# Performance work log

Hardware: AMD Instinct MI355X
Metric: run time of the kernel (lower is better)

The kernel has to match this reference:

```python
import jax, jax.numpy as jnp
import numpy as np

B, T, D, M, W = 512, 2048, 32, 64, 128  # batch, times, data_size, model_size, hidden width


def _linwb(key, out_d, in_d):
    kw, kb = jax.random.split(key)
    s = 1.0 / np.sqrt(in_d)
    return (jax.random.uniform(kw, (out_d, in_d), jnp.float32, -s, s),
            jax.random.uniform(kb, (out_d,), jnp.float32, -s, s))


def setup_inputs() -> dict:
    key = jax.random.key(0)
    ks = jax.random.split(key, 9)
    times = jnp.arange(T, dtype=jnp.float32) / T  # increasing, span [0,1)
    xs = 0.1 * jax.random.normal(ks[0], (B, T, D), jnp.float32)
    # encoder MLP: data_size -> 128 -> 128 -> model_size (relu hidden, identity out; eqx defaults)
    enc_W0, enc_b0 = _linwb(ks[1], W, D)
    enc_W1, enc_b1 = _linwb(ks[2], W, W)
    enc_W2, enc_b2 = _linwb(ks[3], M, W)
    # vector field MLP: model_size -> 128 -> 128 -> model_size*data_size (gelu hidden, tanh out)
    vf_W0, vf_b0 = _linwb(ks[4], W, M)
    vf_W1, vf_b1 = _linwb(ks[5], W, W)
    vf_W2, vf_b2 = _linwb(ks[6], M * D, W)
    # decoder: model_size -> 1 (n_classes==2)
    dec_W, dec_b = _linwb(ks[7], 1, M)
    return dict(times=times, xs=xs,
                enc_W0=enc_W0, enc_b0=enc_b0, enc_W1=enc_W1, enc_b1=enc_b1,
                enc_W2=enc_W2, enc_b2=enc_b2,
                vf_W0=vf_W0, vf_b0=vf_b0, vf_W1=vf_W1, vf_b1=vf_b1,
                vf_W2=vf_W2, vf_b2=vf_b2, dec_W=dec_W, dec_b=dec_b)


def reference(times, xs, enc_W0, enc_b0, enc_W1, enc_b1, enc_W2, enc_b2,
              vf_W0, vf_b0, vf_W1, vf_b1, vf_W2, vf_b2, dec_W, dec_b):
    def encoder(x):  # (B, D) -> (B, M)
        h = jax.nn.relu(x @ enc_W0.T + enc_b0)
        h = jax.nn.relu(h @ enc_W1.T + enc_b1)
        return h @ enc_W2.T + enc_b2

    def vf(y):  # (B, M) -> (B, M, D)
        h = jax.nn.gelu(y @ vf_W0.T + vf_b0)
        h = jax.nn.gelu(h @ vf_W1.T + vf_b1)
        h = jnp.tanh(h @ vf_W2.T + vf_b2)
        return h.reshape(y.shape[0], M, D)

    # Linear interpolation control: dX/dt is piecewise constant on each interval.
    dts = times[1:] - times[:-1]                      # (T-1,)
    dxs = jnp.transpose(xs[:, 1:] - xs[:, :-1], (1, 0, 2))  # (T-1, B, D)

    def step(y, inp):
        dt, dx = inp
        dXdt = dx / dt                                # (B, D)

        def g(y_):  # dy/dt = f(y) @ dX/dt
            return jnp.einsum('bmd,bd->bm', vf(y_), dXdt)

        k1 = g(y)
        k2 = g(y + 0.5 * dt * k1)
        k3 = g(y + 0.5 * dt * k2)
        k4 = g(y + dt * k3)
        return y + (dt / 6.0) * (k1 + 2 * k2 + 2 * k3 + k4), None

    y0 = encoder(xs[:, 0])                            # control.evaluate(t0) == xs[:,0]
    yT, _ = jax.lax.scan(step, y0, (dts, dxs))
    logits = yT @ dec_W.T + dec_b                     # (B, 1)
    return jax.nn.sigmoid(logits)
```

## Files before the change

kernel.cpp:

```cpp
#include <hip/hip_runtime.h>


#define TT   2048
#define NTH  512
#define NCH  8
#define R_P  2
#define L_P  2

typedef _Float16 f16;
typedef _Float16 f16x8 __attribute__((ext_vector_type(8)));
typedef float f32x4 __attribute__((ext_vector_type(4)));

#define O_W2L 0
#define O_DTS 131072
#define O_B2  139264
#define O_H1  147456
#define O_H2  151552
#define O_YIN 155648
#define O_GS  157696
#define O_DX  159744
#define O_B0  160768
#define O_B1  161280
#define LDSB  161792

__device__ __forceinline__ float tanh_fast(float x){
    float e = __expf(2.0f * x);
    return 1.0f - 2.0f * __builtin_amdgcn_rcpf(e + 1.0f);
}
__device__ __forceinline__ float gelu_f(float x){
    float u = x + 0.044715f * x * x * x;
    return 0.5f * x * (1.0f + tanh_fast(0.7978845608028654f * u));
}

template<bool F16>
__device__ __forceinline__ void load_tile_frags(f16x8* buf, const f16* w2r,
                                                const float* vW2, int tl, int l){
    if constexpr (F16){
        const f16* base = w2r + (size_t)tl*2048 + l*8;
        #pragma unroll
        for (int kf = 0; kf < 4; ++kf)
            buf[kf] = *(const f16x8*)(base + kf*512);
    } else {
        int n = tl*16 + (l & 15);
        int k0 = (l >> 4) << 3;
        #pragma unroll
        for (int kf = 0; kf < 4; ++kf){
            const float* p = vW2 + n*128 + kf*32 + k0;
            float4 u = *(const float4*)p;
            float4 v2 = *(const float4*)(p + 4);
            f16x8 t;
            t[0]=(f16)u.x; t[1]=(f16)u.y; t[2]=(f16)u.z; t[3]=(f16)u.w;
            t[4]=(f16)v2.x; t[5]=(f16)v2.y; t[6]=(f16)v2.z; t[7]=(f16)v2.w;
            buf[kf] = t;
        }
    }
}

template<bool F16>
__device__ __forceinline__ void issue_pair(f16x8* de, f16x8* dob, const f16* w2r,
                                           const float* vW2, int w, int p, int l){
    if constexpr (F16){
        const f16* be = w2r + ((size_t)(w*16 + 2*p))*2048 + l*8;
        #pragma unroll
        for (int kf = 0; kf < 4; ++kf){
            de[kf]  = *(const f16x8*)(be + kf*512);
            dob[kf] = *(const f16x8*)(be + 2048 + kf*512);
        }
    } else {
        load_tile_frags<false>(de,  nullptr, vW2, w*16 + 2*p,     l);
        load_tile_frags<false>(dob, nullptr, vW2, w*16 + 2*p + 1, l);
    }
}

__global__ void __launch_bounds__(512) reorder_w2(const float* __restrict__ vW2,
                                                  f16* __restrict__ w2r){
    int idx = blockIdx.x * 512 + threadIdx.x;
    int i  = idx & 7;
    int l  = (idx >> 3) & 63;
    int kf = (idx >> 9) & 3;
    int tl = idx >> 11;
    int n = tl*16 + (l & 15);
    int k = kf*32 + ((l >> 4) << 3) + i;
    w2r[idx] = (f16)vW2[n*128 + k];
}

template<bool F16>
__global__ void __launch_bounds__(NTH, 1)
ncde_main(const float* __restrict__ times, const float* __restrict__ xs,
          const float* __restrict__ eW0, const float* __restrict__ eb0,
          const float* __restrict__ eW1, const float* __restrict__ eb1,
          const float* __restrict__ eW2, const float* __restrict__ eb2,
          const float* __restrict__ vW0, const float* __restrict__ vW1,
          const float* __restrict__ vb0, const float* __restrict__ vb1,
          const float* __restrict__ vW2, const float* __restrict__ vb2,
          const float* __restrict__ dW, const float* __restrict__ db,
          const f16* __restrict__ w2r, float* __restrict__ out)
{
    extern __shared__ __align__(16) char lds[];
    float* dtsf = (float*)(lds + O_DTS);
    float* gsf  = (float*)(lds + O_GS);
    float* dxf  = (float*)(lds + O_DX);
    float* b2s  = (float*)(lds + O_B2);
    float* b0f  = (float*)(lds + O_B0);
    float* b1f  = (float*)(lds + O_B1);
    float* enc1f= (float*)(lds + O_H1);
    float* enc2f= (float*)(lds + O_H2);

    const int tid = threadIdx.x;
    const int l   = tid & 63;
    const int w   = tid >> 6;
    const int c0  = blockIdx.x * NCH;

    for (int i = tid; i < 2047; i += NTH) dtsf[i] = times[i+1] - times[i];
    for (int i = tid; i < 2048; i += NTH) b2s[i] = vb2[i];
    if (tid < 128){ b0f[tid] = vb0[tid]; b1f[tid] = vb1[tid]; }

    float xcur = 0.f, xn = 0.f;
    if (tid < 256){
        int r = tid >> 5, d = tid & 31;
        xcur = xs[((size_t)(c0 + r) * TT + 0) * 32 + d];
        xn   = xs[((size_t)(c0 + r) * TT + 1) * 32 + d];
        dxf[r*32 + d] = xcur;
    }
    __syncthreads();

    for (int i = tid; i < NCH*128; i += NTH){
        int r = i >> 7, n = i & 127;
        float a = eb0[n];
        #pragma unroll
        for (int k = 0; k < 32; ++k) a += eW0[n*32 + k] * dxf[r*32 + k];
        enc1f[i] = fmaxf(a, 0.f);
    }
    __syncthreads();
    for (int i = tid; i < NCH*128; i += NTH){
        int r = i >> 7, n = i & 127;
        float a = eb1[n];
        for (int k = 0; k < 128; ++k) a += eW1[n*128 + k] * enc1f[r*128 + k];
        enc2f[i] = fmaxf(a, 0.f);
    }
    __syncthreads();
    float yreg;
    {
        int r = tid >> 6, m = tid & 63;
        float a = eb2[m];
        for (int k = 0; k < 128; ++k) a += eW2[m*128 + k] * enc2f[r*128 + k];
        yreg = a;
    }
    __syncthreads();

    for (int i = tid; i < 10240/4; i += NTH)
        ((unsigned*)(lds + O_H1))[i] = 0u;
    if constexpr (F16){
        for (int i = tid; i < 8192; i += NTH){
            int slot = i >> 8, b = (i & 255) << 4;
            int sw = slot >> 2, sp = (slot >> 1) & 1, se = slot & 1;
            int tl = sw*16 + 2*(R_P + sp) + se;
            *(f16x8*)(lds + O_W2L + slot*4096 + b) =
                *(const f16x8*)((const char*)w2r + (size_t)tl*4096 + b);
        }
    } else {
        for (int i = tid; i < 65536; i += NTH){
            int slot = i >> 11, elem = i & 2047;
            int sw = slot >> 2, sp = (slot >> 1) & 1, se = slot & 1;
            int tl = sw*16 + 2*(R_P + sp) + se;
            int kf = elem >> 9, rem = elem & 511, ll = rem >> 3, ii = rem & 7;
            int n = tl*16 + (ll & 15);
            int k = kf*32 + ((ll >> 4) << 3) + ii;
            *(f16*)(lds + O_W2L + slot*4096 + elem*2) = (f16)vW2[n*128 + k];
        }
    }
    __syncthreads();

    {
        int r = tid >> 6, m = tid & 63;
        *(f16*)(lds + O_YIN + r*128 + ((m*2) ^ ((r & 7) << 4))) = (f16)yreg;
    }

    f16x8 w0f[2], w1f[4];
    {
        int col  = w*16 + (l & 15);
        int krow = (l >> 4) << 3;
        #pragma unroll
        for (int ks = 0; ks < 2; ++ks){
            const float* p = vW0 + col*64 + ks*32 + krow;
            f16x8 v;
            #pragma unroll
            for (int i = 0; i < 8; ++i) v[i] = (f16)p[i];
            w0f[ks] = v;
        }
        #pragma unroll
        for (int ks = 0; ks < 4; ++ks){
            const float* p = vW1 + col*128 + ks*32 + krow;
            f16x8 v;
            #pragma unroll
            for (int i = 0; i < 8; ++i) v[i] = (f16)p[i];
            w1f[ks] = v;
        }
    }
    f16x8 rw2[R_P][2][4];
    #pragma unroll
    for (int p = 0; p < R_P; ++p)
        #pragma unroll
        for (int e = 0; e < 2; ++e)
            load_tile_frags<F16>(rw2[p][e], w2r, vW2, w*16 + 2*p + e, l);
    __syncthreads();

    const int arow = l & 15;
    const int g    = l >> 4;

    for (int t = 0; t < TT-1; ++t){
        float dtv = dtsf[t];
        float xf = 0.f;
        if (tid < 256){
            int r = tid >> 5, d = tid & 31;
            if (t + 2 < TT) xf = xs[((size_t)(c0 + r) * TT + (t+2)) * 32 + d];
            dxf[r*32 + d] = (xn - xcur) / dtv;
            xcur = xn;
        }
        float ka = 0.f;

        #pragma unroll 1
        for (int st = 0; st < 4; ++st){
            f16x8 sAe[4], sAo[4], sBe[4], sBo[4];
            issue_pair<F16>(sAe, sAo, w2r, vW2, w, 4, l);
            issue_pair<F16>(sBe, sBo, w2r, vW2, w, 5, l);

            {
                f32x4 acc = {0.f,0.f,0.f,0.f};
                #pragma unroll
                for (int kf = 0; kf < 2; ++kf){
                    f16x8 a = *(const f16x8*)(lds + O_YIN + arow*128 +
                               ((kf*64 + g*16) ^ ((arow & 7) << 4)));
                    acc = __builtin_amdgcn_mfma_f32_16x16x32_f16(a, w0f[kf], acc, 0, 0, 0);
                }
                if (g < 2){
                    int col = w*16 + (l & 15);
                    float bb = b0f[col];
                    #pragma unroll
                    for (int j = 0; j < 4; ++j){
                        int row = g*4 + j;
                        float gg = gelu_f(acc[j] + bb);
                        *(f16*)(lds + O_H1 + row*256 + ((col*2) ^ ((row & 7) << 4))) = (f16)gg;
                    }
                }
            }
            __syncthreads();
            {
                f32x4 acc = {0.f,0.f,0.f,0.f};
                #pragma unroll
                for (int kf = 0; kf < 4; ++kf){
                    f16x8 a = *(const f16x8*)(lds + O_H1 + arow*256 +
                               ((kf*64 + g*16) ^ ((arow & 7) << 4)));
                    acc = __builtin_amdgcn_mfma_f32_16x16x32_f16(a, w1f[kf], acc, 0, 0, 0);
                }
                if (g < 2){
                    int col = w*16 + (l & 15);
                    float bb = b1f[col];
                    #pragma unroll
                    for (int j = 0; j < 4; ++j){
                        int row = g*4 + j;
                        float gg = gelu_f(acc[j] + bb);
                        *(f16*)(lds + O_H2 + row*256 + ((col*2) ^ ((row & 7) << 4))) = (f16)gg;
                    }
                }
            }
            __syncthreads();
            {
                f16x8 a3[4];
                #pragma unroll
                for (int kf = 0; kf < 4; ++kf)
                    a3[kf] = *(const f16x8*)(lds + O_H2 + arow*256 +
                              ((kf*64 + g*16) ^ ((arow & 7) << 4)));

                #pragma unroll
                for (int p = 0; p < 8; ++p){
                    f16x8 fe[4], fo[4];
                    if (p < R_P){
                        #pragma unroll
                        for (int kf = 0; kf < 4; ++kf){ fe[kf] = rw2[p][0][kf]; fo[kf] = rw2[p][1][kf]; }
                    } else if (p < R_P + L_P){
                        int slotb = O_W2L + (w*4 + (p - R_P)*2) * 4096 + l*16;
                        #pragma unroll
                        for (int kf = 0; kf < 4; ++kf){
                            fe[kf] = *(const f16x8*)(lds + slotb + kf*1024);
                            fo[kf] = *(const f16x8*)(lds + slotb + 4096 + kf*1024);
                        }
                    } else if (p == 4 || p == 6){
                        #pragma unroll
                        for (int kf = 0; kf < 4; ++kf){ fe[kf] = sAe[kf]; fo[kf] = sAo[kf]; }
                    } else {
                        #pragma unroll
                        for (int kf = 0; kf < 4; ++kf){ fe[kf] = sBe[kf]; fo[kf] = sBo[kf]; }
                    }
                    f32x4 ae = {0.f,0.f,0.f,0.f}, ao = {0.f,0.f,0.f,0.f};
                    #pragma unroll
                    for (int kf = 0; kf < 4; ++kf){
                        ae = __builtin_amdgcn_mfma_f32_16x16x32_f16(a3[kf], fe[kf], ae, 0, 0, 0);
                        ao = __builtin_amdgcn_mfma_f32_16x16x32_f16(a3[kf], fo[kf], ao, 0, 0, 0);
                    }
                    if (p == 4) issue_pair<F16>(sAe, sAo, w2r, vW2, w, 6, l);
                    if (p == 5) issue_pair<F16>(sBe, sBo, w2r, vW2, w, 7, l);
                    {
                        int c   = l & 15;
                        float be = b2s[(w*16 + 2*p)*16 + c];
                        float bo = b2s[(w*16 + 2*p + 1)*16 + c];
                        #pragma unroll
                        for (int j = 0; j < 4; ++j){
                            int rr = (g*4 + j) & 7;
                            float de = dxf[rr*32 + c];
                            float dd = dxf[rr*32 + 16 + c];
                            float pe = tanh_fast(ae[j] + be) * de
                                     + tanh_fast(ao[j] + bo) * dd;
                            pe += __shfl_xor(pe, 1);
                            pe += __shfl_xor(pe, 2);
                            pe += __shfl_xor(pe, 4);
                            pe += __shfl_xor(pe, 8);
                            if (g < 2 && c == p)
                                gsf[(g*4 + j)*64 + w*8 + p] = pe;
                        }
                    }
                }
            }
            __syncthreads();
            {
                int r = tid >> 6, m = tid & 63;
                float kv = gsf[tid];
                float wgt = (st == 1 || st == 2) ? 2.f : 1.f;
                ka += wgt * kv;
                float yst;
                if (st < 3){
                    float cs = (st == 2) ? 1.0f : 0.5f;
                    yst = yreg + cs * dtv * kv;
                } else {
                    yreg = yreg + (dtv * (1.0f/6.0f)) * ka;
                    yst = yreg;
                }
                *(f16*)(lds + O_YIN + r*128 + ((m*2) ^ ((r & 7) << 4))) = (f16)yst;
            }
            __syncthreads();
        }
        if (tid < 256) xn = xf;
    }

    gsf[tid] = yreg * dW[tid & 63];
    __syncthreads();
    if (tid < NCH){
        float a = db[0];
        for (int m = 0; m < 64; ++m) a += gsf[tid*64 + m];
        out[c0 + tid] = 1.0f / (1.0f + __expf(-a));
    }
}

extern "C" void kernel_launch(void* const* d_in, const int* in_sizes, int n_in,
                              void* d_out, int out_size, void* d_ws, size_t ws_size,
                              hipStream_t stream)
{
    const float* times = (const float*)d_in[0];
    const float* xs    = (const float*)d_in[1];
    const float* eW0   = (const float*)d_in[2];
    const float* eb0   = (const float*)d_in[3];
    const float* eW1   = (const float*)d_in[4];
    const float* eb1   = (const float*)d_in[5];
    const float* eW2   = (const float*)d_in[6];
    const float* eb2   = (const float*)d_in[7];
    const float* vW0   = (const float*)d_in[8];
    const float* vb0   = (const float*)d_in[9];
    const float* vW1   = (const float*)d_in[10];
    const float* vb1   = (const float*)d_in[11];
    const float* vW2   = (const float*)d_in[12];
    const float* vb2   = (const float*)d_in[13];
    const float* dW    = (const float*)d_in[14];
    const float* db    = (const float*)d_in[15];

    const size_t w2_bytes = (size_t)2048 * 128 * sizeof(f16);
    if (ws_size >= w2_bytes){
        f16* w2r = (f16*)d_ws;
        reorder_w2<<<dim3(512), dim3(512), 0, stream>>>(vW2, w2r);
        hipFuncSetAttribute((const void*)ncde_main<true>,
                            hipFuncAttributeMaxDynamicSharedMemorySize, LDSB);
        ncde_main<true><<<dim3(64), dim3(NTH), LDSB, stream>>>(
            times, xs, eW0, eb0, eW1, eb1, eW2, eb2,
            vW0, vW1, vb0, vb1, vW2, vb2, dW, db,
            (const f16*)w2r, (float*)d_out);
    } else {
        hipFuncSetAttribute((const void*)ncde_main<false>,
                            hipFuncAttributeMaxDynamicSharedMemorySize, LDSB);
        ncde_main<false><<<dim3(64), dim3(NTH), LDSB, stream>>>(
            times, xs, eW0, eb0, eW1, eb1, eW2, eb2,
            vW0, vW1, vb0, vb1, vW2, vb2, dW, db,
            (const f16*)nullptr, (float*)d_out);
    }
}
```

Before: 81.28 ms.

## Keep RK4 state in MFMA A-fragment registers and drop per-stage barrier

Each lane now holds its slice of the state y and the RK accumulator directly in the MFMA A-operand layout. Stage inputs are rebuilt in registers from the gathered k values, so the YIN LDS buffer and the trailing barrier of every RK stage go away. The dX/dt table is transposed so each lane loads its increments once per timestep as vectors, and the k-value scratch is XOR-swizzled. Plain __syncthreads is replaced by a lightweight lgkmcnt wait plus s_barrier. The cost is redundant per-lane state updates (16 values per lane), more registers and tighter reliance on correct LDS ordering.

```diff
diff --git a/kernel.cpp b/kernel.cpp
--- a/kernel.cpp
+++ b/kernel.cpp
@@ -16,12 +16,11 @@
 #define O_B2  139264
 #define O_H1  147456
 #define O_H2  151552
-#define O_YIN 155648
-#define O_GS  157696
-#define O_DX  159744
-#define O_B0  160768
-#define O_B1  161280
-#define LDSB  161792
+#define O_GS  155648
+#define O_DX  157696
+#define O_B0  158720
+#define O_B1  159232
+#define LDSB  159744
 
 __device__ __forceinline__ float tanh_fast(float x){
     float e = __expf(2.0f * x);
@@ -30,6 +29,11 @@
 __device__ __forceinline__ float gelu_f(float x){
     float u = x + 0.044715f * x * x * x;
     return 0.5f * x * (1.0f + tanh_fast(0.7978845608028654f * u));
+}
+__device__ __forceinline__ void bar_lds(){
+    asm volatile("s_waitcnt lgkmcnt(0)" ::: "memory");
+    __builtin_amdgcn_s_barrier();
+    __builtin_amdgcn_sched_barrier(0);
 }
 
 template<bool F16>
@@ -55,7 +59,6 @@
         }
     }
 }
-
 template<bool F16>
 __device__ __forceinline__ void issue_pair(f16x8* de, f16x8* dob, const f16* w2r,
                                            const float* vW2, int w, int p, int l){
@@ -139,17 +142,43 @@
         enc2f[i] = fmaxf(a, 0.f);
     }
     __syncthreads();
-    float yreg;
+    float y0;
     {
         int r = tid >> 6, m = tid & 63;
         float a = eb2[m];
         for (int k = 0; k < 128; ++k) a += eW2[m*128 + k] * enc2f[r*128 + k];
-        yreg = a;
-    }
-    __syncthreads();
-
-    for (int i = tid; i < 10240/4; i += NTH)
+        y0 = a;
+    }
+    __syncthreads();
+
+    for (int i = tid; i < 8192/4; i += NTH)
         ((unsigned*)(lds + O_H1))[i] = 0u;
+    {
+        int r = tid >> 6, m = tid & 63;
+        gsf[r*64 + (m ^ (r << 3))] = y0;
+    }
+    __syncthreads();
+
+    const int g    = l >> 4;
+    const int arow = l & 15;
+    const int ridx = l & 7;
+    const int c    = l & 15;
+
+    float y_r[16], ka_r[16];
+    f16x8 ah[2];
+    #pragma unroll
+    for (int kf = 0; kf < 2; ++kf){
+        int off = O_GS + ridx*256 + ((((kf<<2)+g) ^ ridx) << 5);
+        f32x4 a = *(const f32x4*)(lds + off);
+        f32x4 b = *(const f32x4*)(lds + off + 16);
+        #pragma unroll
+        for (int i = 0; i < 4; ++i){ y_r[kf*8+i] = a[i]; y_r[kf*8+4+i] = b[i]; }
+        f16x8 h;
+        #pragma unroll
+        for (int i = 0; i < 8; ++i) h[i] = (f16)y_r[kf*8+i];
+        ah[kf] = h;
+    }
+
     if constexpr (F16){
         for (int i = tid; i < 8192; i += NTH){
             int slot = i >> 8, b = (i & 255) << 4;
@@ -169,17 +198,11 @@
             *(f16*)(lds + O_W2L + slot*4096 + elem*2) = (f16)vW2[n*128 + k];
         }
     }
-    __syncthreads();
-
-    {
-        int r = tid >> 6, m = tid & 63;
-        *(f16*)(lds + O_YIN + r*128 + ((m*2) ^ ((r & 7) << 4))) = (f16)yreg;
-    }
 
     f16x8 w0f[2], w1f[4];
     {
-        int col  = w*16 + (l & 15);
-        int krow = (l >> 4) << 3;
+        int col  = w*16 + c;
+        int krow = g << 3;
         #pragma unroll
         for (int ks = 0; ks < 2; ++ks){
             const float* p = vW0 + col*64 + ks*32 + krow;
@@ -205,19 +228,26 @@
             load_tile_frags<F16>(rw2[p][e], w2r, vW2, w*16 + 2*p + e, l);
     __syncthreads();
 
-    const int arow = l & 15;
-    const int g    = l >> 4;
-
     for (int t = 0; t < TT-1; ++t){
         float dtv = dtsf[t];
         float xf = 0.f;
         if (tid < 256){
             int r = tid >> 5, d = tid & 31;
             if (t + 2 < TT) xf = xs[((size_t)(c0 + r) * TT + (t+2)) * 32 + d];
-            dxf[r*32 + d] = (xn - xcur) / dtv;
+            dxf[d*8 + r] = (xn - xcur) / dtv;
             xcur = xn;
         }
-        float ka = 0.f;
+        #pragma unroll
+        for (int i = 0; i < 16; ++i) ka_r[i] = 0.f;
+        bar_lds();
+        float dxe[4], dxd[4];
+        {
+            int rowblk4 = (g & 1) << 4;
+            f32x4 v0 = *(const f32x4*)(lds + O_DX + c*32 + rowblk4);
+            f32x4 v1 = *(const f32x4*)(lds + O_DX + (c+16)*32 + rowblk4);
+            #pragma unroll
+            for (int j = 0; j < 4; ++j){ dxe[j] = v0[j]; dxd[j] = v1[j]; }
+        }
 
         #pragma unroll 1
         for (int st = 0; st < 4; ++st){
@@ -228,13 +258,10 @@
             {
                 f32x4 acc = {0.f,0.f,0.f,0.f};
                 #pragma unroll
-                for (int kf = 0; kf < 2; ++kf){
-                    f16x8 a = *(const f16x8*)(lds + O_YIN + arow*128 +
-                               ((kf*64 + g*16) ^ ((arow & 7) << 4)));
-                    acc = __builtin_amdgcn_mfma_f32_16x16x32_f16(a, w0f[kf], acc, 0, 0, 0);
-                }
+                for (int kf = 0; kf < 2; ++kf)
+                    acc = __builtin_amdgcn_mfma_f32_16x16x32_f16(ah[kf], w0f[kf], acc, 0, 0, 0);
                 if (g < 2){
-                    int col = w*16 + (l & 15);
+                    int col = w*16 + c;
                     float bb = b0f[col];
                     #pragma unroll
                     for (int j = 0; j < 4; ++j){
@@ -244,7 +271,7 @@
                     }
                 }
             }
-            __syncthreads();
+            bar_lds();
             {
                 f32x4 acc = {0.f,0.f,0.f,0.f};
                 #pragma unroll
@@ -254,7 +281,7 @@
                     acc = __builtin_amdgcn_mfma_f32_16x16x32_f16(a, w1f[kf], acc, 0, 0, 0);
                 }
                 if (g < 2){
-                    int col = w*16 + (l & 15);
+                    int col = w*16 + c;
                     float bb = b1f[col];
                     #pragma unroll
                     for (int j = 0; j < 4; ++j){
@@ -264,7 +291,7 @@
                     }
                 }
             }
-            __syncthreads();
+            bar_lds();
             {
                 f16x8 a3[4];
                 #pragma unroll
@@ -301,52 +328,74 @@
                     if (p == 4) issue_pair<F16>(sAe, sAo, w2r, vW2, w, 6, l);
                     if (p == 5) issue_pair<F16>(sBe, sBo, w2r, vW2, w, 7, l);
                     {
-                        int c   = l & 15;
                         float be = b2s[(w*16 + 2*p)*16 + c];
                         float bo = b2s[(w*16 + 2*p + 1)*16 + c];
                         #pragma unroll
                         for (int j = 0; j < 4; ++j){
-                            int rr = (g*4 + j) & 7;
-                            float de = dxf[rr*32 + c];
-                            float dd = dxf[rr*32 + 16 + c];
-                            float pe = tanh_fast(ae[j] + be) * de
-                                     + tanh_fast(ao[j] + bo) * dd;
+                            float pe = tanh_fast(ae[j] + be) * dxe[j]
+                                     + tanh_fast(ao[j] + bo) * dxd[j];
                             pe += __shfl_xor(pe, 1);
                             pe += __shfl_xor(pe, 2);
                             pe += __shfl_xor(pe, 4);
                             pe += __shfl_xor(pe, 8);
-                            if (g < 2 && c == p)
-                                gsf[(g*4 + j)*64 + w*8 + p] = pe;
+                            if (g < 2 && c == p){
+                                int rr = g*4 + j;
+                                gsf[rr*64 + ((w*8 + p) ^ (rr << 3))] = pe;
+                            }
                         }
                     }
                 }
             }
-            __syncthreads();
+            bar_lds();
             {
-                int r = tid >> 6, m = tid & 63;
-                float kv = gsf[tid];
+                float kv[16];
+                #pragma unroll
+                for (int kf = 0; kf < 2; ++kf){
+                    int off = O_GS + ridx*256 + ((((kf<<2)+g) ^ ridx) << 5);
+                    f32x4 a = *(const f32x4*)(lds + off);
+                    f32x4 b = *(const f32x4*)(lds + off + 16);
+                    #pragma unroll
+                    for (int i = 0; i < 4; ++i){ kv[kf*8+i] = a[i]; kv[kf*8+4+i] = b[i]; }
+                }
                 float wgt = (st == 1 || st == 2) ? 2.f : 1.f;
-                ka += wgt * kv;
-                float yst;
+                float ys[16];
+                #pragma unroll
+                for (int i = 0; i < 16; ++i) ka_r[i] += wgt * kv[i];
                 if (st < 3){
-                    float cs = (st == 2) ? 1.0f : 0.5f;
-                    yst = yreg + cs * dtv * kv;
+                    float cs = (st == 2) ? dtv : 0.5f*dtv;
+                    #pragma unroll
+                    for (int i = 0; i < 16; ++i) ys[i] = y_r[i] + cs * kv[i];
                 } else {
-                    yreg = yreg + (dtv * (1.0f/6.0f)) * ka;
-                    yst = yreg;
-                }
-                *(f16*)(lds + O_YIN + r*128 + ((m*2) ^ ((r & 7) << 4))) = (f16)yst;
+                    #pragma unroll
+                    for (int i = 0; i < 16; ++i){ y_r[i] += (dtv*(1.0f/6.0f)) * ka_r[i]; ys[i] = y_r[i]; }
+                }
+                #pragma unroll
+                for (int kf = 0; kf < 2; ++kf){
+                    f16x8 h;
+                    #pragma unroll
+                    for (int i = 0; i < 8; ++i) h[i] = (f16)ys[kf*8+i];
+                    ah[kf] = h;
+                }
             }
-            __syncthreads();
         }
         if (tid < 256) xn = xf;
     }
 
-    gsf[tid] = yreg * dW[tid & 63];
+    __syncthreads();
+    if (arow < 8){
+        #pragma unroll
+        for (int kf = 0; kf < 2; ++kf){
+            f32x4 a, b;
+            #pragma unroll
+            for (int i = 0; i < 4; ++i){ a[i] = y_r[kf*8+i]; b[i] = y_r[kf*8+4+i]; }
+            *(f32x4*)(&gsf[arow*64 + kf*32 + g*8])     = a;
+            *(f32x4*)(&gsf[arow*64 + kf*32 + g*8 + 4]) = b;
+        }
+    }
     __syncthreads();
     if (tid < NCH){
         float a = db[0];
-        for (int m = 0; m < 64; ++m) a += gsf[tid*64 + m];
+        for (int m = 0; m < 64; ++m) a += gsf[tid*64 + m] * dW[m];
         out[c0 + tid] = 1.0f / (1.0f + __expf(-a));
     }
 }
```

New measurement: 127.8 ms. +57.3%, slower.
